# Performance work log

Measured on AMD Instinct MI355X. Metric: run time of the kernel, lower is better.

The kernel has to match this reference:

```python
import jax, jax.numpy as jnp
import numpy as np

K = 7          # kernel_size
PAD = 3        # (dilation*(K-1)+1)//2
EPS = 1e-5     # BatchNorm eps
B, CIN, H, W = 4, 256, 56, 56
CR = 32        # rel_planes
COUT = 256     # out_planes
SP = 8         # share_planes
HN = COUT // SP  # attention heads = 32
OFFS = [(dy, dx) for dy in range(K) for dx in range(K)]


def setup_inputs() -> dict:
    key = jax.random.key(0)
    ks = jax.random.split(key, 24)
    def n(i, shape, s=0.05):
        return jax.random.normal(ks[i], shape, dtype=jnp.float32) * s
    def pos(i, shape):  # positive values for BN gamma / running var
        return jax.random.uniform(ks[i], shape, dtype=jnp.float32, minval=0.5, maxval=1.5)
    return {
        "x": jax.random.normal(ks[0], (B, CIN, H, W), dtype=jnp.float32),
        "w1c": n(1, (CR, CIN)),  "b1c": n(2, (CR,)),
        "w2c": n(3, (CR, CIN)),  "b2c": n(4, (CR,)),
        "w3c": n(5, (COUT, CIN)), "b3c": n(6, (COUT,)),
        "bn1_g": pos(7, (CR,)), "bn1_b": n(8, (CR,)), "bn1_m": n(9, (CR,)), "bn1_v": pos(10, (CR,)),
        "cw1": n(11, (CR, CR)),
        "bn2_g": pos(12, (CR,)), "bn2_b": n(13, (CR,)), "bn2_m": n(14, (CR,)), "bn2_v": pos(15, (CR,)),
        "cw2": n(16, (HN, CR)), "cw2_b": n(17, (HN,)),
    }


def _conv1x1(x, w, b):
    # x: [B,C,H,W], w: [O,C]
    return jnp.einsum('bchw,oc->bohw', x, w) + b[None, :, None, None]


def _bn(y, g, b, m, v):
    # inference BatchNorm2d over channel axis 1; y is 4D
    inv = g / jnp.sqrt(v + EPS)
    return y * inv[None, :, None, None] + (b - m * inv)[None, :, None, None]


def reference(x, w1c, b1c, w2c, b2c, w3c, b3c,
              bn1_g, bn1_b, bn1_m, bn1_v, cw1,
              bn2_g, bn2_b, bn2_m, bn2_v, cw2, cw2_b):
    x1 = _conv1x1(x, w1c, b1c)   # [B,CR,H,W]  query
    x2 = _conv1x1(x, w2c, b2c)   # [B,CR,H,W]  key
    x3 = _conv1x1(x, w3c, b3c)   # [B,COUT,H,W] value

    # Subtraction2 with reflection padding (pad_mode=1):
    # diff[b,c,k,i] = x1[b,c,i] - patch_k(x2)[b,c,i]
    x2p = jnp.pad(x2, ((0, 0), (0, 0), (PAD, PAD), (PAD, PAD)), mode='reflect')
    diff = jnp.stack([x1 - x2p[:, :, dy:dy + H, dx:dx + W] for dy, dx in OFFS],
                     axis=2)                      # [B,CR,49,H,W]
    diff = diff.reshape(B, CR, K * K, H * W)      # [B,CR,49,HW]

    # conv_w: BN -> ReLU -> 1x1 conv (no bias) -> BN -> ReLU -> 1x1 conv
    y = jax.nn.relu(_bn(diff, bn1_g, bn1_b, bn1_m, bn1_v))
    y = jnp.einsum('bkln,ok->boln', y, cw1)       # [B,CR,49,HW]
    y = jax.nn.relu(_bn(y, bn2_g, bn2_b, bn2_m, bn2_v))
    logits = jnp.einsum('bkln,ok->boln', y, cw2) + cw2_b[None, :, None, None]
    wgt = jax.nn.softmax(logits, axis=2)          # softmax over k^2, [B,HN,49,HW]
    wgt = wgt.reshape(B, HN, K * K, H, W)

    # Aggregation with reflection padding: out[b,c,i] = sum_k patch_k(x3)[b,c,i] * w[b,c//SP,k,i]
    x3p = jnp.pad(x3, ((0, 0), (0, 0), (PAD, PAD), (PAD, PAD)), mode='reflect')
    out = jnp.zeros((B, HN, SP, H, W), dtype=x.dtype)
    for k, (dy, dx) in enumerate(OFFS):
        patch = x3p[:, :, dy:dy + H, dx:dx + W].reshape(B, HN, SP, H, W)
        out = out + patch * wgt[:, :, k][:, :, None]
    return out.reshape(B, COUT, H, W)
```

## Files before the change

kernel.cpp:

```cpp
#include <hip/hip_runtime.h>
#include <math.h>

#define HW_N   3136
#define W_DIM  56
#define C_IN   256
#define C_R    32
#define C_OUT  256
#define C_ALL  320
#define K2D    49
#define RS     40
#define BN_EPS 1e-5f

typedef _Float16 h2 __attribute__((ext_vector_type(2)));
typedef _Float16 h4 __attribute__((ext_vector_type(4)));
typedef __fp16  g2 __attribute__((ext_vector_type(2)));
typedef __fp16  g4 __attribute__((ext_vector_type(4)));
typedef __fp16  g8 __attribute__((ext_vector_type(8)));
typedef float   f4 __attribute__((ext_vector_type(4)));

__device__ __forceinline__ h2 pkrtz(float a, float b) {
    g2 r = __builtin_amdgcn_cvt_pkrtz(a, b);
    return __builtin_bit_cast(h2, r);
}

__device__ __forceinline__ g8 pack8(float4 a, float4 b) {
    g2 p0 = __builtin_amdgcn_cvt_pkrtz(a.x, a.y);
    g2 p1 = __builtin_amdgcn_cvt_pkrtz(a.z, a.w);
    g2 p2 = __builtin_amdgcn_cvt_pkrtz(b.x, b.y);
    g2 p3 = __builtin_amdgcn_cvt_pkrtz(b.z, b.w);
    g8 o;
    o[0] = p0[0]; o[1] = p0[1]; o[2] = p1[0]; o[3] = p1[1];
    o[4] = p2[0]; o[5] = p2[1]; o[6] = p3[0]; o[7] = p3[1];
    return o;
}

__device__ __forceinline__ int refl(int v) {
    v = (v < 0) ? -v : v;
    return (v > 55) ? (110 - v) : v;
}

__device__ __forceinline__ void wave_fence() {
    asm volatile("s_waitcnt lgkmcnt(0)" ::: "memory");
}

__global__ __launch_bounds__(256) void k_conv_mfma(
    const float* __restrict__ x,
    const float* __restrict__ w1c, const float* __restrict__ w2c,
    const float* __restrict__ w3c,
    const float* __restrict__ b1c, const float* __restrict__ b2c,
    const float* __restrict__ b3c, __fp16* __restrict__ xall16)
{
    __shared__ __align__(16) _Float16 smem[32 * 328];
    const int t = threadIdx.x, w = t >> 6, lane = t & 63;
    const int quad = lane >> 4, l16 = lane & 15;
    const int b = blockIdx.z, pos0 = blockIdx.x * 32;

    {
        const int p = t & 31;
        const int gb = t >> 5;
        const float* xp = x + (size_t)b * C_IN * HW_N + pos0 + p;
#pragma unroll
        for (int i = 0; i < 4; ++i) {
            const int g = i * 8 + gb;
            const int ci = g * 8;
            float v[8];
#pragma unroll
            for (int j = 0; j < 8; ++j) v[j] = xp[(size_t)(ci + j) * HW_N];
            g8 o;
#pragma unroll
            for (int jj = 0; jj < 4; ++jj) {
                const g2 pr = __builtin_amdgcn_cvt_pkrtz(v[2 * jj], v[2 * jj + 1]);
                o[2 * jj] = pr[0]; o[2 * jj + 1] = pr[1];
            }
            *(g8*)((__fp16*)smem + (size_t)(p * 32 + (g ^ (p & 7))) * 8) = o;
        }
    }
    __syncthreads();

    const float* wrow[5]; float bias[5];
#pragma unroll
    for (int nt = 0; nt < 5; ++nt) {
        const int co = w * 80 + nt * 16 + l16;
        wrow[nt] = (co < 32) ? (w1c + co * C_IN)
                 : (co < 64) ? (w2c + (co - 32) * C_IN)
                             : (w3c + (co - 64) * C_IN);
        bias[nt] = (co < 32) ? b1c[co] : (co < 64) ? b2c[co - 32] : b3c[co - 64];
    }

    f4 acc[2][5];
#pragma unroll
    for (int mt = 0; mt < 2; ++mt)
#pragma unroll
        for (int nt = 0; nt < 5; ++nt) acc[mt][nt] = (f4){0.f, 0.f, 0.f, 0.f};

    const int xo = l16 & 7;
#pragma unroll
    for (int ks = 0; ks < 8; ++ks) {
        g8 bf[5];
#pragma unroll
        for (int nt = 0; nt < 5; ++nt) {
            const float* wp = wrow[nt] + ks * 32 + quad * 8;
            bf[nt] = pack8(*(const float4*)wp, *(const float4*)(wp + 4));
        }
#pragma unroll
        for (int mt = 0; mt < 2; ++mt) {
            const int row = mt * 16 + l16;
            const g8 af = *(const g8*)((const __fp16*)smem
                          + (size_t)(row * 32 + ((ks * 4 + quad) ^ xo)) * 8);
#pragma unroll
            for (int nt = 0; nt < 5; ++nt)
                acc[mt][nt] = __builtin_amdgcn_mfma_f32_16x16x32_f16(af, bf[nt], acc[mt][nt], 0, 0, 0);
        }
    }
    __syncthreads();

#pragma unroll
    for (int mt = 0; mt < 2; ++mt)
#pragma unroll
        for (int nt = 0; nt < 5; ++nt) {
            const int co = w * 80 + nt * 16 + l16;
#pragma unroll
            for (int r = 0; r < 4; ++r) {
                const int row = mt * 16 + quad * 4 + r;
                smem[row * 328 + co] = (_Float16)(acc[mt][nt][r] + bias[nt]);
            }
        }
    __syncthreads();
#pragma unroll
    for (int i = 0; i < 5; ++i) {
        const int idx = i * 256 + t;
        const int row = idx / 40, c8 = idx - row * 40;
        const g8 v = *(const g8*)((const __fp16*)smem + row * 328 + c8 * 8);
        *(g8*)(xall16 + ((size_t)b * HW_N + pos0 + row) * C_ALL + c8 * 8) = v;
    }
}

__global__ __launch_bounds__(256) void k_attn(
    const __fp16* __restrict__ xq,
    const float* __restrict__ bn1_g, const float* __restrict__ bn1_b,
    const float* __restrict__ bn1_m, const float* __restrict__ bn1_v,
    const float* __restrict__ cw1,
    const float* __restrict__ bn2_g, const float* __restrict__ bn2_b,
    const float* __restrict__ bn2_m, const float* __restrict__ bn2_v,
    const float* __restrict__ cw2, const float* __restrict__ cw2_b,
    float* __restrict__ out)
{
    __shared__ __align__(16) _Float16 tbuf[4][64 * RS];
    __shared__ int pk[4][52];
    const int tid = threadIdx.x;
    const int w = tid >> 6, lane = tid & 63;
    const int b = blockIdx.y;
    const int bid  = blockIdx.x;
    const int posb = (bid & 7) * 98 + (bid >> 3);
    const int pos0 = posb * 4;
    const int pos  = pos0 + w;
    const int y0 = pos / W_DIM, x0 = pos - y0 * W_DIM;
    const __fp16* __restrict__ base16 = xq + (size_t)b * HW_N * C_ALL;
    _Float16* tb = tbuf[w];
    float* stage_w = (float*)(tb + 49 * RS);

    {
        const int c4 = lane & 7;
        const int kh = lane >> 3;
        const float4 g  = *(const float4*)(bn1_g + 4 * c4);
        const float4 bb = *(const float4*)(bn1_b + 4 * c4);
        const float4 m  = *(const float4*)(bn1_m + 4 * c4);
        const float4 v  = *(const float4*)(bn1_v + 4 * c4);
        const float iv0 = g.x * rsqrtf(v.x + BN_EPS), bt0 = bb.x - m.x * iv0;
        const float iv1 = g.y * rsqrtf(v.y + BN_EPS), bt1 = bb.y - m.y * iv1;
        const float iv2 = g.z * rsqrtf(v.z + BN_EPS), bt2 = bb.z - m.z * iv2;
        const float iv3 = g.w * rsqrtf(v.w + BN_EPS), bt3 = bb.w - m.w * iv3;
        const g4 x1p = *(const g4*)(base16 + (size_t)pos * C_ALL + 4 * c4);
        const float x1a = (float)x1p[0], x1b = (float)x1p[1];
        const float x1c = (float)x1p[2], x1d = (float)x1p[3];
#pragma unroll
        for (int j = 0; j < 7; ++j) {
            const int k = 8 * j + kh;
            if (k < K2D) {
                const int dy = k / 7, dx = k - dy * 7;
                const int rp = refl(y0 + dy - 3) * W_DIM + refl(x0 + dx - 3);
                if (c4 == 0) pk[w][k] = rp;
                const g4 x2p = *(const g4*)(base16 + (size_t)rp * C_ALL + 32 + 4 * c4);
                const float t0 = fmaxf((x1a - (float)x2p[0]) * iv0 + bt0, 0.f);
                const float t1 = fmaxf((x1b - (float)x2p[1]) * iv1 + bt1, 0.f);
                const float t2 = fmaxf((x1c - (float)x2p[2]) * iv2 + bt2, 0.f);
                const float t3 = fmaxf((x1d - (float)x2p[3]) * iv3 + bt3, 0.f);
                const h2 lo = pkrtz(t0, t1), hi = pkrtz(t2, t3);
                h4 tt; tt[0] = lo[0]; tt[1] = lo[1]; tt[2] = hi[0]; tt[3] = hi[1];
                *(h4*)&tb[k * RS + 4 * c4] = tt;
            }
        }
    }
    wave_fence();

    const int quad = lane >> 4, l16 = lane & 15;
    f4 acc[4][2];

    {
        g8 bf[2];
#pragma unroll
        for (int nt = 0; nt < 2; ++nt) {
            const float* wr = cw1 + (nt * 16 + l16) * C_R + quad * 8;
            bf[nt] = pack8(*(const float4*)wr, *(const float4*)(wr + 4));
        }
#pragma unroll
        for (int mt = 0; mt < 4; ++mt) {
            acc[mt][0] = (f4){0.f, 0.f, 0.f, 0.f};
            acc[mt][1] = (f4){0.f, 0.f, 0.f, 0.f};
            const g8 af = *(const g8*)((const __fp16*)tb + (mt * 16 + l16) * RS + quad * 8);
            acc[mt][0] = __builtin_amdgcn_mfma_f32_16x16x32_f16(af, bf[0], acc[mt][0], 0, 0, 0);
            acc[mt][1] = __builtin_amdgcn_mfma_f32_16x16x32_f16(af, bf[1], acc[mt][1], 0, 0, 0);
        }
    }
    wave_fence();

#pragma unroll
    for (int nt = 0; nt < 2; ++nt) {
        const int o = nt * 16 + l16;
        const float iv = bn2_g[o] * rsqrtf(bn2_v[o] + BN_EPS);
        const float bt = bn2_b[o] - bn2_m[o] * iv;
#pragma unroll
        for (int mt = 0; mt < 4; ++mt)
#pragma unroll
            for (int r = 0; r < 4; ++r) {
                const int row = mt * 16 + quad * 4 + r;
                tb[row * RS + o] = (_Float16)fmaxf(acc[mt][nt][r] * iv + bt, 0.f);
            }
    }
    wave_fence();

    {
        g8 bf[2];
#pragma unroll
        for (int nt = 0; nt < 2; ++nt) {
            const float* wr = cw2 + (nt * 16 + l16) * C_R + quad * 8;
            bf[nt] = pack8(*(const float4*)wr, *(const float4*)(wr + 4));
        }
#pragma unroll
        for (int mt = 0; mt < 4; ++mt) {
            acc[mt][0] = (f4){0.f, 0.f, 0.f, 0.f};
            acc[mt][1] = (f4){0.f, 0.f, 0.f, 0.f};
            const g8 af = *(const g8*)((const __fp16*)tb + (mt * 16 + l16) * RS + quad * 8);
            acc[mt][0] = __builtin_amdgcn_mfma_f32_16x16x32_f16(af, bf[0], acc[mt][0], 0, 0, 0);
            acc[mt][1] = __builtin_amdgcn_mfma_f32_16x16x32_f16(af, bf[1], acc[mt][1], 0, 0, 0);
        }
    }
    wave_fence();

#pragma unroll
    for (int nt = 0; nt < 2; ++nt) {
        const float bsv = cw2_b[nt * 16 + l16];
        float m = -1e30f;
#pragma unroll
        for (int mt = 0; mt < 4; ++mt)
#pragma unroll
            for (int r = 0; r < 4; ++r) {
                const int k = mt * 16 + quad * 4 + r;
                const float v = acc[mt][nt][r] + bsv;
                acc[mt][nt][r] = v;
                if (k < K2D) m = fmaxf(m, v);
            }
        m = fmaxf(m, __shfl_xor(m, 16, 64));
        m = fmaxf(m, __shfl_xor(m, 32, 64));
        float s = 0.f;
#pragma unroll
        for (int mt = 0; mt < 4; ++mt)
#pragma unroll
            for (int r = 0; r < 4; ++r) {
                const int k = mt * 16 + quad * 4 + r;
                const float e = (k < K2D) ? __expf(acc[mt][nt][r] - m) : 0.f;
                acc[mt][nt][r] = e;
                s += e;
            }
        s += __shfl_xor(s, 16, 64);
        s += __shfl_xor(s, 32, 64);
        const float rs = 1.f / s;
        const int o = nt * 16 + l16;
#pragma unroll
        for (int mt = 0; mt < 4; ++mt)
#pragma unroll
            for (int r = 0; r < 4; ++r) {
                const int row = mt * 16 + quad * 4 + r;
                if (row < K2D)
                    tb[row * RS + o] = (_Float16)(acc[mt][nt][r] * rs);
            }
    }
    wave_fence();

    {
        const int hn = lane >> 1;
        float4 a = make_float4(0.f, 0.f, 0.f, 0.f);
#pragma unroll 7
        for (int k = 0; k < K2D; ++k) {
            const int rp = pk[w][k];
            const float wv = (float)tb[k * RS + hn];
            const g4 v = *(const g4*)(base16 + (size_t)rp * C_ALL + 64 + lane * 4);
            a.x += (float)v[0] * wv; a.y += (float)v[1] * wv;
            a.z += (float)v[2] * wv; a.w += (float)v[3] * wv;
        }
        *(float4*)&stage_w[lane * 4] = a;
    }
    __syncthreads();

    {
        const int c = tid;
        const float* st0 = (const float*)(tbuf[0] + 49 * RS);
        const float* st1 = (const float*)(tbuf[1] + 49 * RS);
        const float* st2 = (const float*)(tbuf[2] + 49 * RS);
        const float* st3 = (const float*)(tbuf[3] + 49 * RS);
        float4 o;
        o.x = st0[c]; o.y = st1[c];
        o.z = st2[c]; o.w = st3[c];
        *(float4*)(out + ((size_t)b * C_OUT + c) * HW_N + pos0) = o;
    }
}

extern "C" void kernel_launch(void* const* d_in, const int* in_sizes, int n_in,
                              void* d_out, int out_size, void* d_ws, size_t ws_size,
                              hipStream_t stream)
{
    const float* x     = (const float*)d_in[0];
    const float* w1c   = (const float*)d_in[1];
    const float* b1c   = (const float*)d_in[2];
    const float* w2c   = (const float*)d_in[3];
    const float* b2c   = (const float*)d_in[4];
    const float* w3c   = (const float*)d_in[5];
    const float* b3c   = (const float*)d_in[6];
    const float* bn1_g = (const float*)d_in[7];
    const float* bn1_b = (const float*)d_in[8];
    const float* bn1_m = (const float*)d_in[9];
    const float* bn1_v = (const float*)d_in[10];
    const float* cw1   = (const float*)d_in[11];
    const float* bn2_g = (const float*)d_in[12];
    const float* bn2_b = (const float*)d_in[13];
    const float* bn2_m = (const float*)d_in[14];
    const float* bn2_v = (const float*)d_in[15];
    const float* cw2   = (const float*)d_in[16];
    const float* cw2_b = (const float*)d_in[17];

    __fp16* xall16 = (__fp16*)d_ws;

    k_conv_mfma<<<dim3(98, 1, 4), 256, 0, stream>>>(x, w1c, w2c, w3c,
                                                    b1c, b2c, b3c, xall16);
    k_attn<<<dim3(784, 4, 1), 256, 0, stream>>>(xall16,
        bn1_g, bn1_b, bn1_m, bn1_v, cw1,
        bn2_g, bn2_b, bn2_m, bn2_v, cw2, cw2_b, (float*)d_out);
}
```

Before: 156.5 us.

## Process two pixels per wave in attention kernel, halving grid size

Each wave in k_attn now handles two output positions instead of one. Its MFMA, softmax and aggregation loops are interleaved across both pixels, so each block covers 8 positions and the grid shrinks to 392 blocks per batch. The goal is more independent work per wave to hide gather-load latency, fewer blocks to launch, weight fragments shared across pixels, and 32-byte output stores. In exchange the kernel doubles its LDS footprint and its accumulator registers, and adds launch_bounds(256,4), which risks spills or lower occupancy.

After: 160.3 us. 2.5% more time.

```diff
diff --git a/kernel.cpp b/kernel.cpp
--- a/kernel.cpp
+++ b/kernel.cpp
@@ -135,7 +135,7 @@
     }
 }
 
-__global__ __launch_bounds__(256) void k_attn(
+__global__ __launch_bounds__(256, 4) void k_attn(
     const __fp16* __restrict__ xq,
     const float* __restrict__ bn1_g, const float* __restrict__ bn1_b,
     const float* __restrict__ bn1_m, const float* __restrict__ bn1_v,
@@ -145,19 +145,19 @@
     const float* __restrict__ cw2, const float* __restrict__ cw2_b,
     float* __restrict__ out)
 {
-    __shared__ __align__(16) _Float16 tbuf[4][64 * RS];
-    __shared__ int pk[4][52];
+    __shared__ __align__(16) _Float16 tbuf[8][64 * RS];
+    __shared__ int pk[8][52];
     const int tid = threadIdx.x;
     const int w = tid >> 6, lane = tid & 63;
     const int b = blockIdx.y;
     const int bid  = blockIdx.x;
-    const int posb = (bid & 7) * 98 + (bid >> 3);
-    const int pos0 = posb * 4;
-    const int pos  = pos0 + w;
-    const int y0 = pos / W_DIM, x0 = pos - y0 * W_DIM;
+    const int posb = (bid & 7) * 49 + (bid >> 3);
+    const int pos0 = posb * 8;
     const __fp16* __restrict__ base16 = xq + (size_t)b * HW_N * C_ALL;
-    _Float16* tb = tbuf[w];
-    float* stage_w = (float*)(tb + 49 * RS);
+
+    _Float16* tbp[2] = { tbuf[2 * w], tbuf[2 * w + 1] };
+    int* pkp[2] = { pk[2 * w], pk[2 * w + 1] };
+    int posP[2] = { pos0 + 2 * w, pos0 + 2 * w + 1 };
 
     {
         const int c4 = lane & 7;
@@ -170,31 +170,37 @@
         const float iv1 = g.y * rsqrtf(v.y + BN_EPS), bt1 = bb.y - m.y * iv1;
         const float iv2 = g.z * rsqrtf(v.z + BN_EPS), bt2 = bb.z - m.z * iv2;
         const float iv3 = g.w * rsqrtf(v.w + BN_EPS), bt3 = bb.w - m.w * iv3;
-        const g4 x1p = *(const g4*)(base16 + (size_t)pos * C_ALL + 4 * c4);
-        const float x1a = (float)x1p[0], x1b = (float)x1p[1];
-        const float x1c = (float)x1p[2], x1d = (float)x1p[3];
-#pragma unroll
-        for (int j = 0; j < 7; ++j) {
-            const int k = 8 * j + kh;
-            if (k < K2D) {
-                const int dy = k / 7, dx = k - dy * 7;
-                const int rp = refl(y0 + dy - 3) * W_DIM + refl(x0 + dx - 3);
-                if (c4 == 0) pk[w][k] = rp;
-                const g4 x2p = *(const g4*)(base16 + (size_t)rp * C_ALL + 32 + 4 * c4);
-                const float t0 = fmaxf((x1a - (float)x2p[0]) * iv0 + bt0, 0.f);
-                const float t1 = fmaxf((x1b - (float)x2p[1]) * iv1 + bt1, 0.f);
-                const float t2 = fmaxf((x1c - (float)x2p[2]) * iv2 + bt2, 0.f);
-                const float t3 = fmaxf((x1d - (float)x2p[3]) * iv3 + bt3, 0.f);
-                const h2 lo = pkrtz(t0, t1), hi = pkrtz(t2, t3);
-                h4 tt; tt[0] = lo[0]; tt[1] = lo[1]; tt[2] = hi[0]; tt[3] = hi[1];
-                *(h4*)&tb[k * RS + 4 * c4] = tt;
+#pragma unroll
+        for (int p = 0; p < 2; ++p) {
+            const int pos = posP[p];
+            const int y0 = pos / W_DIM, x0 = pos - y0 * W_DIM;
+            _Float16* tb = tbp[p];
+            const g4 x1p = *(const g4*)(base16 + (size_t)pos * C_ALL + 4 * c4);
+            const float x1a = (float)x1p[0], x1b = (float)x1p[1];
+            const float x1c = (float)x1p[2], x1d = (float)x1p[3];
+#pragma unroll
+            for (int j = 0; j < 7; ++j) {
+                const int k = 8 * j + kh;
+                if (k < K2D) {
+                    const int dy = k / 7, dx = k - dy * 7;
+                    const int rp = refl(y0 + dy - 3) * W_DIM + refl(x0 + dx - 3);
+                    if (c4 == 0) pkp[p][k] = rp;
+                    const g4 x2p = *(const g4*)(base16 + (size_t)rp * C_ALL + 32 + 4 * c4);
+                    const float t0 = fmaxf((x1a - (float)x2p[0]) * iv0 + bt0, 0.f);
+                    const float t1 = fmaxf((x1b - (float)x2p[1]) * iv1 + bt1, 0.f);
+                    const float t2 = fmaxf((x1c - (float)x2p[2]) * iv2 + bt2, 0.f);
+                    const float t3 = fmaxf((x1d - (float)x2p[3]) * iv3 + bt3, 0.f);
+                    const h2 lo = pkrtz(t0, t1), hi = pkrtz(t2, t3);
+                    h4 tt; tt[0] = lo[0]; tt[1] = lo[1]; tt[2] = hi[0]; tt[3] = hi[1];
+                    *(h4*)&tb[k * RS + 4 * c4] = tt;
+                }
             }
         }
     }
     wave_fence();
 
     const int quad = lane >> 4, l16 = lane & 15;
-    f4 acc[4][2];
+    f4 acc[2][4][2];
 
     {
         g8 bf[2];
@@ -204,13 +210,15 @@
             bf[nt] = pack8(*(const float4*)wr, *(const float4*)(wr + 4));
         }
 #pragma unroll
-        for (int mt = 0; mt < 4; ++mt) {
-            acc[mt][0] = (f4){0.f, 0.f, 0.f, 0.f};
-            acc[mt][1] = (f4){0.f, 0.f, 0.f, 0.f};
-            const g8 af = *(const g8*)((const __fp16*)tb + (mt * 16 + l16) * RS + quad * 8);
-            acc[mt][0] = __builtin_amdgcn_mfma_f32_16x16x32_f16(af, bf[0], acc[mt][0], 0, 0, 0);
-            acc[mt][1] = __builtin_amdgcn_mfma_f32_16x16x32_f16(af, bf[1], acc[mt][1], 0, 0, 0);
-        }
+        for (int p = 0; p < 2; ++p)
+#pragma unroll
+            for (int mt = 0; mt < 4; ++mt) {
+                acc[p][mt][0] = (f4){0.f, 0.f, 0.f, 0.f};
+                acc[p][mt][1] = (f4){0.f, 0.f, 0.f, 0.f};
+                const g8 af = *(const g8*)((const __fp16*)tbp[p] + (mt * 16 + l16) * RS + quad * 8);
+                acc[p][mt][0] = __builtin_amdgcn_mfma_f32_16x16x32_f16(af, bf[0], acc[p][mt][0], 0, 0, 0);
+                acc[p][mt][1] = __builtin_amdgcn_mfma_f32_16x16x32_f16(af, bf[1], acc[p][mt][1], 0, 0, 0);
+            }
     }
     wave_fence();
 
@@ -220,12 +228,14 @@
         const float iv = bn2_g[o] * rsqrtf(bn2_v[o] + BN_EPS);
         const float bt = bn2_b[o] - bn2_m[o] * iv;
 #pragma unroll
-        for (int mt = 0; mt < 4; ++mt)
-#pragma unroll
-            for (int r = 0; r < 4; ++r) {
-                const int row = mt * 16 + quad * 4 + r;
-                tb[row * RS + o] = (_Float16)fmaxf(acc[mt][nt][r] * iv + bt, 0.f);
-            }
+        for (int p = 0; p < 2; ++p)
+#pragma unroll
+            for (int mt = 0; mt < 4; ++mt)
+#pragma unroll
+                for (int r = 0; r < 4; ++r) {
+                    const int row = mt * 16 + quad * 4 + r;
+                    tbp[p][row * RS + o] = (_Float16)fmaxf(acc[p][mt][nt][r] * iv + bt, 0.f);
+                }
     }
     wave_fence();
 
@@ -237,81 +247,100 @@
             bf[nt] = pack8(*(const float4*)wr, *(const float4*)(wr + 4));
         }
 #pragma unroll
-        for (int mt = 0; mt < 4; ++mt) {
-            acc[mt][0] = (f4){0.f, 0.f, 0.f, 0.f};
-            acc[mt][1] = (f4){0.f, 0.f, 0.f, 0.f};
-            const g8 af = *(const g8*)((const __fp16*)tb + (mt * 16 + l16) * RS + quad * 8);
-            acc[mt][0] = __builtin_amdgcn_mfma_f32_16x16x32_f16(af, bf[0], acc[mt][0], 0, 0, 0);
-            acc[mt][1] = __builtin_amdgcn_mfma_f32_16x16x32_f16(af, bf[1], acc[mt][1], 0, 0, 0);
-        }
-    }
-    wave_fence();
-
-#pragma unroll
-    for (int nt = 0; nt < 2; ++nt) {
-        const float bsv = cw2_b[nt * 16 + l16];
-        float m = -1e30f;
-#pragma unroll
-        for (int mt = 0; mt < 4; ++mt)
-#pragma unroll
-            for (int r = 0; r < 4; ++r) {
-                const int k = mt * 16 + quad * 4 + r;
-                const float v = acc[mt][nt][r] + bsv;
-                acc[mt][nt][r] = v;
-                if (k < K2D) m = fmaxf(m, v);
-            }
-        m = fmaxf(m, __shfl_xor(m, 16, 64));
-        m = fmaxf(m, __shfl_xor(m, 32, 64));
-        float s = 0.f;
-#pragma unroll
-        for (int mt = 0; mt < 4; ++mt)
-#pragma unroll
-            for (int r = 0; r < 4; ++r) {
-                const int k = mt * 16 + quad * 4 + r;
-                const float e = (k < K2D) ? __expf(acc[mt][nt][r] - m) : 0.f;
-                acc[mt][nt][r] = e;
-                s += e;
-            }
-        s += __shfl_xor(s, 16, 64);
-        s += __shfl_xor(s, 32, 64);
-        const float rs = 1.f / s;
-        const int o = nt * 16 + l16;
-#pragma unroll
-        for (int mt = 0; mt < 4; ++mt)
-#pragma unroll
-            for (int r = 0; r < 4; ++r) {
-                const int row = mt * 16 + quad * 4 + r;
-                if (row < K2D)
-                    tb[row * RS + o] = (_Float16)(acc[mt][nt][r] * rs);
-            }
-    }
+        for (int p = 0; p < 2; ++p)
+#pragma unroll
+            for (int mt = 0; mt < 4; ++mt) {
+                acc[p][mt][0] = (f4){0.f, 0.f, 0.f, 0.f};
+                acc[p][mt][1] = (f4){0.f, 0.f, 0.f, 0.f};
+                const g8 af = *(const g8*)((const __fp16*)tbp[p] + (mt * 16 + l16) * RS + quad * 8);
+                acc[p][mt][0] = __builtin_amdgcn_mfma_f32_16x16x32_f16(af, bf[0], acc[p][mt][0], 0, 0, 0);
+                acc[p][mt][1] = __builtin_amdgcn_mfma_f32_16x16x32_f16(af, bf[1], acc[p][mt][1], 0, 0, 0);
+            }
+    }
+    wave_fence();
+
+#pragma unroll
+    for (int p = 0; p < 2; ++p)
+#pragma unroll
+        for (int nt = 0; nt < 2; ++nt) {
+            const float bsv = cw2_b[nt * 16 + l16];
+            float m = -1e30f;
+#pragma unroll
+            for (int mt = 0; mt < 4; ++mt)
+#pragma unroll
+                for (int r = 0; r < 4; ++r) {
+                    const int k = mt * 16 + quad * 4 + r;
+                    const float v = acc[p][mt][nt][r] + bsv;
+                    acc[p][mt][nt][r] = v;
+                    if (k < K2D) m = fmaxf(m, v);
+                }
+            m = fmaxf(m, __shfl_xor(m, 16, 64));
+            m = fmaxf(m, __shfl_xor(m, 32, 64));
+            float s = 0.f;
+#pragma unroll
+            for (int mt = 0; mt < 4; ++mt)
+#pragma unroll
+                for (int r = 0; r < 4; ++r) {
+                    const int k = mt * 16 + quad * 4 + r;
+                    const float e = (k < K2D) ? __expf(acc[p][mt][nt][r] - m) : 0.f;
+                    acc[p][mt][nt][r] = e;
+                    s += e;
+                }
+            s += __shfl_xor(s, 16, 64);
+            s += __shfl_xor(s, 32, 64);
+            const float rs = 1.f / s;
+            const int o = nt * 16 + l16;
+#pragma unroll
+            for (int mt = 0; mt < 4; ++mt)
+#pragma unroll
+                for (int r = 0; r < 4; ++r) {
+                    const int row = mt * 16 + quad * 4 + r;
+                    if (row < K2D)
+                        tbp[p][row * RS + o] = (_Float16)(acc[p][mt][nt][r] * rs);
+                }
+        }
     wave_fence();
 
     {
         const int hn = lane >> 1;
-        float4 a = make_float4(0.f, 0.f, 0.f, 0.f);
+        const __fp16* x3p = base16 + 64 + lane * 4;
+        const _Float16* tA = tbp[0];
+        const _Float16* tB = tbp[1];
+        const int* pkA = pkp[0];
+        const int* pkB = pkp[1];
+        float4 aA = make_float4(0.f, 0.f, 0.f, 0.f);
+        float4 aB = make_float4(0.f, 0.f, 0.f, 0.f);
 #pragma unroll 7
         for (int k = 0; k < K2D; ++k) {
-            const int rp = pk[w][k];
-            const float wv = (float)tb[k * RS + hn];
-            const g4 v = *(const g4*)(base16 + (size_t)rp * C_ALL + 64 + lane * 4);
-            a.x += (float)v[0] * wv; a.y += (float)v[1] * wv;
-            a.z += (float)v[2] * wv; a.w += (float)v[3] * wv;
-        }
-        *(float4*)&stage_w[lane * 4] = a;
+            const int rpA = pkA[k], rpB = pkB[k];
+            const float wvA = (float)tA[k * RS + hn];
+            const float wvB = (float)tB[k * RS + hn];
+            const g4 vA = *(const g4*)(x3p + (size_t)rpA * C_ALL);
+            const g4 vB = *(const g4*)(x3p + (size_t)rpB * C_ALL);
+            aA.x += (float)vA[0] * wvA; aA.y += (float)vA[1] * wvA;
+            aA.z += (float)vA[2] * wvA; aA.w += (float)vA[3] * wvA;
+            aB.x += (float)vB[0] * wvB; aB.y += (float)vB[1] * wvB;
+            aB.z += (float)vB[2] * wvB; aB.w += (float)vB[3] * wvB;
+        }
+        *(float4*)((float*)(tA + 49 * RS) + lane * 4) = aA;
+        *(float4*)((float*)(tB + 49 * RS) + lane * 4) = aB;
     }
     __syncthreads();
 
     {
         const int c = tid;
-        const float* st0 = (const float*)(tbuf[0] + 49 * RS);
-        const float* st1 = (const float*)(tbuf[1] + 49 * RS);
-        const float* st2 = (const float*)(tbuf[2] + 49 * RS);
-        const float* st3 = (const float*)(tbuf[3] + 49 * RS);
-        float4 o;
-        o.x = st0[c]; o.y = st1[c];
-        o.z = st2[c]; o.w = st3[c];
-        *(float4*)(out + ((size_t)b * C_OUT + c) * HW_N + pos0) = o;
+        float4 o0, o1;
+        o0.x = ((const float*)(tbuf[0] + 49 * RS))[c];
+        o0.y = ((const float*)(tbuf[1] + 49 * RS))[c];
+        o0.z = ((const float*)(tbuf[2] + 49 * RS))[c];
+        o0.w = ((const float*)(tbuf[3] + 49 * RS))[c];
+        o1.x = ((const float*)(tbuf[4] + 49 * RS))[c];
+        o1.y = ((const float*)(tbuf[5] + 49 * RS))[c];
+        o1.z = ((const float*)(tbuf[6] + 49 * RS))[c];
+        o1.w = ((const float*)(tbuf[7] + 49 * RS))[c];
+        float* op = out + ((size_t)b * C_OUT + c) * HW_N + pos0;
+        *(float4*)op = o0;
+        *(float4*)(op + 4) = o1;
     }
 }
 
@@ -342,7 +371,7 @@
 
     k_conv_mfma<<<dim3(98, 1, 4), 256, 0, stream>>>(x, w1c, w2c, w3c,
                                                     b1c, b2c, b3c, xall16);
-    k_attn<<<dim3(784, 4, 1), 256, 0, stream>>>(xall16,
+    k_attn<<<dim3(392, 4, 1), 256, 0, stream>>>(xall16,
         bn1_g, bn1_b, bn1_m, bn1_v, cw1,
         bn2_g, bn2_b, bn2_m, bn2_v, cw2, cw2_b, (float*)d_out);
 }
```
